# Performance work log

Hardware: AMD Instinct MI355X
Metric: run time of the kernel (lower is better)

## Reference

```python
import jax, jax.numpy as jnp
import numpy as np
from jax import lax

NCLASSES = 3
NMS_PRE = 100
NMS_THR = 0.01
SCORE_THR = 0.1
MAX_NUM = 50
H, W = 248, 216
BS = 16


def make_anchors():
    # Faithful to Anchors(ranges, sizes, rotations) in __init__.
    z0s = np.array([-0.6, -0.6, -1.78], np.float32)
    sizes = np.array([[0.6, 0.8, 1.73], [0.6, 1.76, 1.73], [1.6, 3.9, 1.56]], np.float32)
    rotations = np.array([0.0, 1.57], np.float32)
    x = (np.arange(W, dtype=np.float32) + 0.5) * (69.12 / W)
    y = (np.arange(H, dtype=np.float32) + 0.5) * (79.36 / H) - 39.68
    yy, xx = np.meshgrid(y, x, indexing='ij')  # (H, W)
    anchors = np.zeros((H, W, 3, 2, 7), np.float32)
    for c in range(3):
        for r in range(2):
            anchors[:, :, c, r, 0] = xx
            anchors[:, :, c, r, 1] = yy
            anchors[:, :, c, r, 2] = z0s[c]
            anchors[:, :, c, r, 3:6] = sizes[c]
            anchors[:, :, c, r, 6] = rotations[r]
    return jnp.asarray(anchors)


def setup_inputs() -> dict:
    key = jax.random.key(0)
    k1, k2, k3 = jax.random.split(key, 3)
    return {
        'bbox_cls_pred': jax.random.normal(k1, (BS, 18, H, W), jnp.float32),
        'bbox_pred': jax.random.normal(k2, (BS, 42, H, W), jnp.float32) * 0.1,
        'bbox_dir_cls_pred': jax.random.normal(k3, (BS, 12, H, W), jnp.float32),
        'anchors': make_anchors(),
    }


def limit_period(val, offset=1.0, period=np.pi):
    return val - jnp.floor(val / period + offset) * period


def anchors2bboxes(anchors, deltas):
    xa, ya, za, wa, la, ha, ra = [anchors[:, i] for i in range(7)]
    dx, dy, dz, dw, dl, dh, dr = [deltas[:, i] for i in range(7)]
    da = jnp.sqrt(wa * wa + la * la)
    x = dx * da + xa
    y = dy * da + ya
    z = dz * ha + za + ha * 0.5
    w = wa * jnp.exp(dw)
    l = la * jnp.exp(dl)
    h = ha * jnp.exp(dh)
    z = z - h * 0.5
    theta = ra + dr
    return jnp.stack([x, y, z, w, l, h, theta], axis=-1)


def nms_keep(boxes2d, scores, valid, thresh):
    # Greedy NMS over fixed NMS_PRE boxes; invalid boxes never kept / never suppress.
    n = scores.shape[0]
    order = jnp.argsort(-jnp.where(valid, scores, -jnp.inf))
    b = boxes2d[order]
    v = valid[order]
    area = (b[:, 2] - b[:, 0]) * (b[:, 3] - b[:, 1])
    x1 = jnp.maximum(b[:, None, 0], b[None, :, 0])
    y1 = jnp.maximum(b[:, None, 1], b[None, :, 1])
    x2 = jnp.minimum(b[:, None, 2], b[None, :, 2])
    y2 = jnp.minimum(b[:, None, 3], b[None, :, 3])
    inter = jnp.maximum(x2 - x1, 0.0) * jnp.maximum(y2 - y1, 0.0)
    iou = inter / (area[:, None] + area[None, :] - inter + 1e-8)
    idx = jnp.arange(n)
    def body(i, keep):
        sup = (iou[i] > thresh) & (idx > i) & keep[i]
        return keep & ~sup
    keep = lax.fori_loop(0, n, body, v)
    return jnp.zeros(n, bool).at[order].set(keep)


def process_single(cls_pred, box_pred, dir_pred, anchors):
    # cls_pred (18,H,W), box_pred (42,H,W), dir_pred (12,H,W), anchors (H,W,3,2,7)
    cls = jnp.transpose(cls_pred, (1, 2, 0)).reshape(-1, NCLASSES)
    box = jnp.transpose(box_pred, (1, 2, 0)).reshape(-1, 7)
    dirp = jnp.transpose(dir_pred, (1, 2, 0)).reshape(-1, 2)
    anc = anchors.reshape(-1, 7)
    cls = jax.nn.sigmoid(cls)
    dir_cls = jnp.argmax(dirp, axis=1)
    _, inds = lax.top_k(jnp.max(cls, axis=1), NMS_PRE)
    cls = cls[inds]
    box = box[inds]
    dir_cls = dir_cls[inds]
    anc = anc[inds]
    bboxes = anchors2bboxes(anc, box)  # (NMS_PRE, 7): x,y,z,w,l,h,theta
    xy = bboxes[:, :2]
    wl = bboxes[:, 3:5]
    boxes2d = jnp.concatenate([xy - wl / 2, xy + wl / 2], axis=-1)
    # Torch code detaches theta through limit_period; dir term is constant.
    theta = lax.stop_gradient(limit_period(bboxes[:, 6])) + (1.0 - dir_cls.astype(bboxes.dtype)) * np.pi
    bboxes = bboxes.at[:, 6].set(theta)
    keeps = []
    for c in range(NCLASSES):
        sc = cls[:, c]
        valid = sc > SCORE_THR
        keeps.append(nms_keep(boxes2d, sc, valid, NMS_THR) & valid)
    keep = jnp.stack(keeps)            # (3, NMS_PRE)
    scores_all = cls.T                 # (3, NMS_PRE)
    flat = jnp.where(keep, scores_all, -1.0).reshape(-1)
    final_scores, fi = lax.top_k(flat, MAX_NUM)
    sel = fi % NMS_PRE
    labels = fi // NMS_PRE
    out_bboxes = bboxes[sel]
    mask = final_scores > 0.0
    return out_bboxes, labels, final_scores, mask


def reference(bbox_cls_pred, bbox_pred, bbox_dir_cls_pred, anchors):
    f = jax.vmap(process_single, in_axes=(0, 0, 0, None))
    return f(bbox_cls_pred, bbox_pred, bbox_dir_cls_pred, anchors)
```

## Files before the change

kernel.cpp:

```cpp
#include <hip/hip_runtime.h>
#include <cstdint>

#pragma clang fp contract(off)

#define HH 248
#define WW 216
#define HW (HH*WW)
#define NROW (6*HW)
#define BATCH 16
#define NPRE 100
#define MAXNUM 50
#define NB 2048
#define CAP 2048
#define SBLK 53
#define K0 64
#define NSLOT (SBLK*K0)
#define QMAX 14
#define PIF 3.14159274101257324f

#define T0BKT 1966u
#define FBINS (NB - (int)T0BKT)

#define CNTB_OFF 0
#define KEYS_OFF 3584

__device__ __forceinline__ float sigmoidf_ref(float x) {
    if (x >= 0.0f) {
        return 1.0f / (1.0f + expf(-x));
    } else {
        float e = expf(x);
        return e / (1.0f + e);
    }
}

__device__ __forceinline__ unsigned bucket_of(unsigned bits) {
    unsigned b = (bits >= 0x3F000000u) ? (1024u + ((bits - 0x3F000000u) >> 13))
                                       : (bits >> 20);
    return (b > (unsigned)(NB - 1)) ? (unsigned)(NB - 1) : b;
}

__device__ __forceinline__ void emit_one(unsigned bits, unsigned row,
                                         unsigned* lcnt,
                                         unsigned long long* kseg) {
    if (bucket_of(bits) >= T0BKT) {
        unsigned pos = atomicAdd(lcnt, 1u);
        if (pos < (unsigned)K0)
            kseg[pos] = ((unsigned long long)bits << 32) |
                        (unsigned long long)(0xFFFFFFFFu - row);
    }
}

__global__ __launch_bounds__(256) void k_score(const float* __restrict__ cls,
                                               unsigned* __restrict__ cntB,
                                               unsigned long long* __restrict__ keys) {
    int t = threadIdx.x, blk = blockIdx.x, b = blockIdx.y;
    __shared__ unsigned lcnt;
    if (t == 0) lcnt = 0;
    __syncthreads();

    unsigned long long* kseg = keys + (size_t)(b * SBLK + blk) * K0;
    int cell0 = blk * 1024 + t * 4;
    if (cell0 < HW) {
        const float* p = cls + (size_t)b * 18 * HW;
        #pragma unroll
        for (int a = 0; a < 6; ++a) {
            float4 l0 = *(const float4*)(p + (size_t)(a*3+0)*HW + cell0);
            float4 l1 = *(const float4*)(p + (size_t)(a*3+1)*HW + cell0);
            float4 l2 = *(const float4*)(p + (size_t)(a*3+2)*HW + cell0);
            unsigned b0 = __float_as_uint(sigmoidf_ref(fmaxf(l0.x, fmaxf(l1.x, l2.x))));
            unsigned b1 = __float_as_uint(sigmoidf_ref(fmaxf(l0.y, fmaxf(l1.y, l2.y))));
            unsigned b2 = __float_as_uint(sigmoidf_ref(fmaxf(l0.z, fmaxf(l1.z, l2.z))));
            unsigned b3 = __float_as_uint(sigmoidf_ref(fmaxf(l0.w, fmaxf(l1.w, l2.w))));
            emit_one(b0, (unsigned)((cell0+0)*6 + a), &lcnt, kseg);
            emit_one(b1, (unsigned)((cell0+1)*6 + a), &lcnt, kseg);
            emit_one(b2, (unsigned)((cell0+2)*6 + a), &lcnt, kseg);
            emit_one(b3, (unsigned)((cell0+3)*6 + a), &lcnt, kseg);
        }
    }
    __syncthreads();
    if (t == 0) cntB[b * SBLK + blk] = lcnt;
}

__global__ __launch_bounds__(256) void k_final(
    const float* __restrict__ cls, const float* __restrict__ box,
    const float* __restrict__ dir, const float* __restrict__ anc,
    const unsigned* __restrict__ cntB, const unsigned long long* __restrict__ keys,
    float* __restrict__ out) {
    int b = blockIdx.x, t = threadIdx.x;

    __shared__ unsigned long long keyS[CAP];
    __shared__ int   selRow[NPRE];
    __shared__ float bb[NPRE][7];
    __shared__ float b2d[NPRE][4];
    __shared__ float areaS[NPRE];
    __shared__ float clsS[3][NPRE];
    __shared__ float svalS[3][NPRE];
    __shared__ int   ordS[3][NPRE];
    __shared__ int   rankS[3][NPRE];
    __shared__ float4 sbox[3][NPRE];
    __shared__ float  sarea[3][NPRE];
    __shared__ unsigned keepInit[3][4];
    __shared__ unsigned long long maskS[3][NPRE][2];
    __shared__ unsigned long long keepBits[3][2];
    __shared__ float flatS[3*NPRE];
    __shared__ unsigned fh[FBINS];
    __shared__ unsigned fsuf[FBINS + 1];
    __shared__ unsigned cntS[SBLK];
    __shared__ unsigned slowH[NB];
    __shared__ int  tbS;
    __shared__ unsigned StbS;
    __shared__ int  safeS;
    __shared__ unsigned mcnt;

    if (t == 0) { tbS = -1; StbS = 0; mcnt = 0; }
    if (t < FBINS) fh[t] = 0;
    if (t == FBINS) fsuf[FBINS] = 0;
    if (t < SBLK) cntS[t] = cntB[b * SBLK + t];
    __syncthreads();

    unsigned long long kq[QMAX];
    #pragma unroll
    for (int q = 0; q < QMAX; ++q) {
        unsigned long long kk = 0ULL;
        int s = t + q * 256;
        if (s < NSLOT) {
            int k = s >> 6, i = s & 63;
            if ((unsigned)i < cntS[k])
                kk = keys[(size_t)(b * SBLK + k) * K0 + i];
        }
        kq[q] = kk;
    }

    #pragma unroll
    for (int q = 0; q < QMAX; ++q) {
        unsigned bk = bucket_of((unsigned)(kq[q] >> 32));
        if (bk >= T0BKT) atomicAdd(&fh[bk - T0BKT], 1u);
    }
    __syncthreads();

    if (t < FBINS) {
        unsigned s = 0;
        int j = t;
        for (; j + 3 < FBINS; j += 4)
            s += fh[j] + fh[j+1] + fh[j+2] + fh[j+3];
        for (; j < FBINS; ++j) s += fh[j];
        fsuf[t] = s;
    }
    __syncthreads();
    if (t < FBINS) {
        unsigned S = fsuf[t], Sn = fsuf[t + 1];
        if (S >= (unsigned)NPRE && Sn < (unsigned)NPRE) {
            tbS = (int)T0BKT + t;
            StbS = S;
        }
    }
    __syncthreads();

    if (t < 64) {
        unsigned c = (t < SBLK) ? cntS[t] : 0u;
        unsigned long long ov = __ballot(c > (unsigned)K0);
        if (t == 0)
            safeS = (tbS >= 0) && (ov == 0ULL) && (StbS <= (unsigned)CAP) ? 1 : 0;
    }
    __syncthreads();

    int tb = tbS;
    int M;
    if (safeS) {
        #pragma unroll
        for (int q = 0; q < QMAX; ++q) {
            unsigned long long kk = kq[q];
            if (bucket_of((unsigned)(kk >> 32)) >= (unsigned)tb) {
                unsigned pos = atomicAdd(&mcnt, 1u);
                keyS[pos] = kk;
            }
        }
        __syncthreads();
        M = (int)mcnt;
    } else {
        for (int i = t; i < NB; i += 256) slowH[i] = 0;
        __syncthreads();
        const float* p = cls + (size_t)b * 18 * HW;
        for (int cell = t; cell < HW; cell += 256) {
            for (int a = 0; a < 6; ++a) {
                float v0 = p[(size_t)(a*3+0)*HW + cell];
                float v1 = p[(size_t)(a*3+1)*HW + cell];
                float v2 = p[(size_t)(a*3+2)*HW + cell];
                unsigned bits = __float_as_uint(sigmoidf_ref(fmaxf(v0, fmaxf(v1, v2))));
                atomicAdd(&slowH[bucket_of(bits)], 1u);
            }
        }
        __syncthreads();
        if (t == 0) {
            unsigned cum = 0;
            int r = 0;
            for (int j = NB - 1; j >= 0; --j) {
                cum += slowH[j];
                if (cum >= (unsigned)NPRE) { r = j; break; }
            }
            tbS = r;
        }
        __syncthreads();
        tb = tbS;
        for (int cell = t; cell < HW; cell += 256) {
            for (int a = 0; a < 6; ++a) {
                float v0 = p[(size_t)(a*3+0)*HW + cell];
                float v1 = p[(size_t)(a*3+1)*HW + cell];
                float v2 = p[(size_t)(a*3+2)*HW + cell];
                unsigned bits = __float_as_uint(sigmoidf_ref(fmaxf(v0, fmaxf(v1, v2))));
                if (bucket_of(bits) >= (unsigned)tb) {
                    unsigned pos = atomicAdd(&mcnt, 1u);
                    if (pos < (unsigned)CAP)
                        keyS[pos] = ((unsigned long long)bits << 32) |
                                    (unsigned long long)(0xFFFFFFFFu - (unsigned)(cell*6 + a));
                }
            }
        }
        __syncthreads();
        M = (mcnt < (unsigned)CAP) ? (int)mcnt : CAP;
    }
    __syncthreads();

    for (int i = t; i < M; i += 256) {
        unsigned long long k = keyS[i];
        int r = 0;
        int j = 0;
        for (; j + 3 < M; j += 4) {
            unsigned long long a0 = keyS[j+0], a1 = keyS[j+1];
            unsigned long long a2 = keyS[j+2], a3 = keyS[j+3];
            r += (int)(a0 > k) + (int)(a1 > k) + (int)(a2 > k) + (int)(a3 > k);
        }
        for (; j < M; ++j) r += (int)(keyS[j] > k);
        if (r < NPRE) selRow[r] = (int)(0xFFFFFFFFu - (unsigned)(k & 0xFFFFFFFFull));
    }
    __syncthreads();

    if (t < NPRE) {
        int row = selRow[t];
        int a = row % 6;
        int cell = row / 6;
        const float* cb = cls + (size_t)b * 18 * HW + cell;
        clsS[0][t] = sigmoidf_ref(cb[(size_t)(a*3+0)*HW]);
        clsS[1][t] = sigmoidf_ref(cb[(size_t)(a*3+1)*HW]);
        clsS[2][t] = sigmoidf_ref(cb[(size_t)(a*3+2)*HW]);
        const float* db = dir + (size_t)b * 12 * HW + cell;
        float d0 = db[(size_t)(a*2+0)*HW];
        float d1 = db[(size_t)(a*2+1)*HW];
        int dircls = (d1 > d0) ? 1 : 0;
        const float* pb = box + (size_t)b * 42 * HW + cell;
        float dx = pb[(size_t)(a*7+0)*HW], dy = pb[(size_t)(a*7+1)*HW], dz = pb[(size_t)(a*7+2)*HW];
        float dw = pb[(size_t)(a*7+3)*HW], dl = pb[(size_t)(a*7+4)*HW], dh = pb[(size_t)(a*7+5)*HW];
        float dr = pb[(size_t)(a*7+6)*HW];
        const float* ab = anc + (size_t)row * 7;
        float xa = ab[0], ya = ab[1], za = ab[2];
        float wa = ab[3], la = ab[4], ha = ab[5], ra = ab[6];
        float da = sqrtf(wa*wa + la*la);
        float x = dx*da + xa;
        float y = dy*da + ya;
        float z = dz*ha + za + ha*0.5f;
        float wv = wa*expf(dw);
        float lv = la*expf(dl);
        float hv = ha*expf(dh);
        z = z - hv*0.5f;
        float th0 = ra + dr;
        float lim = th0 - floorf(th0/PIF + 1.0f)*PIF;
        float theta = lim + (1.0f - (float)dircls)*PIF;
        bb[t][0]=x; bb[t][1]=y; bb[t][2]=z; bb[t][3]=wv; bb[t][4]=lv; bb[t][5]=hv; bb[t][6]=theta;
        b2d[t][0] = x - wv*0.5f;
        b2d[t][1] = y - lv*0.5f;
        b2d[t][2] = x + wv*0.5f;
        b2d[t][3] = y + lv*0.5f;
        areaS[t] = (b2d[t][2]-b2d[t][0]) * (b2d[t][3]-b2d[t][1]);
    }
    if (t < 12) keepInit[t/4][t%4] = 0u;
    __syncthreads();

    for (int w = t; w < 3*NPRE; w += 256) {
        int c = w / NPRE, p = w % NPRE;
        float sc = clsS[c][p];
        svalS[c][p] = (sc > 0.1f) ? sc : -INFINITY;
    }
    __syncthreads();

    for (int w = t; w < 3*NPRE; w += 256) {
        int c = w / NPRE, p = w % NPRE;
        float v = svalS[c][p];
        int r = 0;
        for (int j0 = 0; j0 < NPRE; j0 += 4) {
            float v0 = svalS[c][j0+0], v1 = svalS[c][j0+1];
            float v2 = svalS[c][j0+2], v3 = svalS[c][j0+3];
            r += (int)(v0 > v || (v0 == v && (j0+0) < p));
            r += (int)(v1 > v || (v1 == v && (j0+1) < p));
            r += (int)(v2 > v || (v2 == v && (j0+2) < p));
            r += (int)(v3 > v || (v3 == v && (j0+3) < p));
        }
        ordS[c][r] = p;
        rankS[c][p] = r;
        if (v != -INFINITY) atomicOr(&keepInit[c][r >> 5], 1u << (r & 31));
    }
    __syncthreads();

    for (int w = t; w < 3*NPRE; w += 256) {
        int c = w / NPRE, i = w % NPRE;
        int pi = ordS[c][i];
        sbox[c][i] = make_float4(b2d[pi][0], b2d[pi][1], b2d[pi][2], b2d[pi][3]);
        sarea[c][i] = areaS[pi];
    }
    __syncthreads();

    for (int w = t; w < 3*NPRE; w += 256) {
        int c = w / NPRE, i = w % NPRE;
        float4 bi = sbox[c][i];
        float ai = sarea[c][i];
        unsigned long long m0 = 0ULL, m1 = 0ULL;
        #pragma unroll 2
        for (int j = i + 1; j < NPRE; ++j) {
            float4 bj = sbox[c][j];
            float x1 = fmaxf(bi.x, bj.x);
            float y1 = fmaxf(bi.y, bj.y);
            float x2 = fminf(bi.z, bj.z);
            float y2 = fminf(bi.w, bj.w);
            float inter = fmaxf(x2 - x1, 0.0f) * fmaxf(y2 - y1, 0.0f);
            float iou = inter / (ai + sarea[c][j] - inter + 1e-8f);
            unsigned long long hit = (iou > 0.01f) ? 1ULL : 0ULL;
            if (j < 64) m0 |= hit << j;
            else        m1 |= hit << (j - 64);
        }
        maskS[c][i][0] = m0;
        maskS[c][i][1] = m1;
    }
    __syncthreads();

    if (t < 3) {
        int c = t;
        unsigned long long k0 = (unsigned long long)keepInit[c][0] |
                                ((unsigned long long)keepInit[c][1] << 32);
        unsigned long long k1 = (unsigned long long)keepInit[c][2] |
                                ((unsigned long long)keepInit[c][3] << 32);
        unsigned long long todo = k0;
        while (todo) {
            int i = __builtin_ctzll(todo);
            unsigned long long m0 = maskS[c][i][0];
            unsigned long long m1 = maskS[c][i][1];
            k0 &= ~m0;
            k1 &= ~m1;
            todo = (todo & (todo - 1)) & ~m0;
        }
        todo = k1;
        while (todo) {
            int i = __builtin_ctzll(todo);
            unsigned long long m1 = maskS[c][64 + i][1];
            k1 &= ~m1;
            todo = (todo & (todo - 1)) & ~m1;
        }
        keepBits[c][0] = k0;
        keepBits[c][1] = k1;
    }
    __syncthreads();

    for (int w = t; w < 3*NPRE; w += 256) {
        int c = w / NPRE, p = w % NPRE;
        int r = rankS[c][p];
        unsigned long long bit = (r < 64) ? (keepBits[c][0] >> r) : (keepBits[c][1] >> (r - 64));
        flatS[w] = (bit & 1ULL) ? clsS[c][p] : -1.0f;
    }
    __syncthreads();

    for (int i = t; i < 3*NPRE; i += 256) {
        float vi = flatS[i];
        int r2 = 0;
        for (int j0 = 0; j0 < 3*NPRE; j0 += 4) {
            float v0 = flatS[j0+0], v1 = flatS[j0+1];
            float v2 = flatS[j0+2], v3 = flatS[j0+3];
            r2 += (int)(v0 > vi || (v0 == vi && (j0+0) < i));
            r2 += (int)(v1 > vi || (v1 == vi && (j0+1) < i));
            r2 += (int)(v2 > vi || (v2 == vi && (j0+2) < i));
            r2 += (int)(v3 > vi || (v3 == vi && (j0+3) < i));
        }
        if (r2 < MAXNUM) {
            int p = i % NPRE;
            int lab = i / NPRE;
            int o = b * MAXNUM + r2;
            float* ob = out + (size_t)o * 7;
            for (int j = 0; j < 7; ++j) ob[j] = bb[p][j];
            out[BATCH*MAXNUM*7 + o] = (float)lab;
            out[BATCH*MAXNUM*8 + o] = vi;
            out[BATCH*MAXNUM*9 + o] = (vi > 0.0f) ? 1.0f : 0.0f;
        }
    }
}

extern "C" void kernel_launch(void* const* d_in, const int* in_sizes, int n_in,
                              void* d_out, int out_size, void* d_ws, size_t ws_size,
                              hipStream_t stream) {
    const float* cls = (const float*)d_in[0];
    const float* box = (const float*)d_in[1];
    const float* dir = (const float*)d_in[2];
    const float* anc = (const float*)d_in[3];
    float* out = (float*)d_out;
    char* ws = (char*)d_ws;

    unsigned* cntB = (unsigned*)(ws + CNTB_OFF);
    unsigned long long* keys = (unsigned long long*)(ws + KEYS_OFF);

    dim3 g(SBLK, BATCH);
    k_score<<<g, 256, 0, stream>>>(cls, cntB, keys);
    k_final<<<BATCH, 256, 0, stream>>>(cls, box, dir, anc, cntB, keys, out);
}
```

Before: 292.7 us.

## Fuse score scan and final NMS into one kernel with last-block election

```diff
diff --git a/kernel.cpp b/kernel.cpp
--- a/kernel.cpp
+++ b/kernel.cpp
@@ -18,10 +18,11 @@
 #define QMAX 14
 #define PIF 3.14159274101257324f
 
-#define T0BKT 1966u
-#define FBINS (NB - (int)T0BKT)
-
-#define CNTB_OFF 0
+#define XCUT 3.17805383f
+#define FBINS 92
+
+#define DONE_OFF 0
+#define CNTB_OFF 64
 #define KEYS_OFF 3584
 
 __device__ __forceinline__ float sigmoidf_ref(float x) {
@@ -39,54 +40,20 @@
     return (b > (unsigned)(NB - 1)) ? (unsigned)(NB - 1) : b;
 }
 
-__device__ __forceinline__ void emit_one(unsigned bits, unsigned row,
-                                         unsigned* lcnt,
-                                         unsigned long long* kseg) {
-    if (bucket_of(bits) >= T0BKT) {
-        unsigned pos = atomicAdd(lcnt, 1u);
-        if (pos < (unsigned)K0)
-            kseg[pos] = ((unsigned long long)bits << 32) |
-                        (unsigned long long)(0xFFFFFFFFu - row);
-    }
+__device__ __forceinline__ int lbin(unsigned bits, unsigned x0) {
+    if (bits < x0) return -1;
+    unsigned d = (bits - x0) >> 17;
+    return (d > (unsigned)(FBINS - 1)) ? (FBINS - 1) : (int)d;
 }
 
-__global__ __launch_bounds__(256) void k_score(const float* __restrict__ cls,
-                                               unsigned* __restrict__ cntB,
-                                               unsigned long long* __restrict__ keys) {
-    int t = threadIdx.x, blk = blockIdx.x, b = blockIdx.y;
-    __shared__ unsigned lcnt;
-    if (t == 0) lcnt = 0;
-    __syncthreads();
-
-    unsigned long long* kseg = keys + (size_t)(b * SBLK + blk) * K0;
-    int cell0 = blk * 1024 + t * 4;
-    if (cell0 < HW) {
-        const float* p = cls + (size_t)b * 18 * HW;
-        #pragma unroll
-        for (int a = 0; a < 6; ++a) {
-            float4 l0 = *(const float4*)(p + (size_t)(a*3+0)*HW + cell0);
-            float4 l1 = *(const float4*)(p + (size_t)(a*3+1)*HW + cell0);
-            float4 l2 = *(const float4*)(p + (size_t)(a*3+2)*HW + cell0);
-            unsigned b0 = __float_as_uint(sigmoidf_ref(fmaxf(l0.x, fmaxf(l1.x, l2.x))));
-            unsigned b1 = __float_as_uint(sigmoidf_ref(fmaxf(l0.y, fmaxf(l1.y, l2.y))));
-            unsigned b2 = __float_as_uint(sigmoidf_ref(fmaxf(l0.z, fmaxf(l1.z, l2.z))));
-            unsigned b3 = __float_as_uint(sigmoidf_ref(fmaxf(l0.w, fmaxf(l1.w, l2.w))));
-            emit_one(b0, (unsigned)((cell0+0)*6 + a), &lcnt, kseg);
-            emit_one(b1, (unsigned)((cell0+1)*6 + a), &lcnt, kseg);
-            emit_one(b2, (unsigned)((cell0+2)*6 + a), &lcnt, kseg);
-            emit_one(b3, (unsigned)((cell0+3)*6 + a), &lcnt, kseg);
-        }
-    }
-    __syncthreads();
-    if (t == 0) cntB[b * SBLK + blk] = lcnt;
-}
-
-__global__ __launch_bounds__(256) void k_final(
+__global__ __launch_bounds__(256) void k_fused(
     const float* __restrict__ cls, const float* __restrict__ box,
     const float* __restrict__ dir, const float* __restrict__ anc,
-    const unsigned* __restrict__ cntB, const unsigned long long* __restrict__ keys,
+    unsigned* __restrict__ doneCnt, unsigned* __restrict__ cntB,
+    unsigned long long* __restrict__ keys,
     float* __restrict__ out) {
-    int b = blockIdx.x, t = threadIdx.x;
+    int t = threadIdx.x, blk = blockIdx.x, b = blockIdx.y;
+    const unsigned x0 = __float_as_uint(XCUT);
 
     __shared__ unsigned long long keyS[CAP];
     __shared__ int   selRow[NPRE];
@@ -111,6 +78,62 @@
     __shared__ unsigned StbS;
     __shared__ int  safeS;
     __shared__ unsigned mcnt;
+    __shared__ unsigned lcnt;
+    __shared__ int  amLastS;
+
+    if (t == 0) lcnt = 0;
+    __syncthreads();
+
+    unsigned long long* kseg = keys + (size_t)(b * SBLK + blk) * K0;
+    int cell0 = blk * 1024 + t * 4;
+    if (cell0 < HW) {
+        const float* p = cls + (size_t)b * 18 * HW;
+        #pragma unroll
+        for (int a = 0; a < 6; ++a) {
+            float4 l0 = *(const float4*)(p + (size_t)(a*3+0)*HW + cell0);
+            float4 l1 = *(const float4*)(p + (size_t)(a*3+1)*HW + cell0);
+            float4 l2 = *(const float4*)(p + (size_t)(a*3+2)*HW + cell0);
+            float m0 = fmaxf(l0.x, fmaxf(l1.x, l2.x));
+            float m1 = fmaxf(l0.y, fmaxf(l1.y, l2.y));
+            float m2 = fmaxf(l0.z, fmaxf(l1.z, l2.z));
+            float m3 = fmaxf(l0.w, fmaxf(l1.w, l2.w));
+            if (m0 >= XCUT) {
+                unsigned pos = atomicAdd(&lcnt, 1u);
+                if (pos < (unsigned)K0)
+                    kseg[pos] = ((unsigned long long)__float_as_uint(m0) << 32) |
+                                (unsigned long long)(0xFFFFFFFFu - (unsigned)((cell0+0)*6 + a));
+            }
+            if (m1 >= XCUT) {
+                unsigned pos = atomicAdd(&lcnt, 1u);
+                if (pos < (unsigned)K0)
+                    kseg[pos] = ((unsigned long long)__float_as_uint(m1) << 32) |
+                                (unsigned long long)(0xFFFFFFFFu - (unsigned)((cell0+1)*6 + a));
+            }
+            if (m2 >= XCUT) {
+                unsigned pos = atomicAdd(&lcnt, 1u);
+                if (pos < (unsigned)K0)
+                    kseg[pos] = ((unsigned long long)__float_as_uint(m2) << 32) |
+                                (unsigned long long)(0xFFFFFFFFu - (unsigned)((cell0+2)*6 + a));
+            }
+            if (m3 >= XCUT) {
+                unsigned pos = atomicAdd(&lcnt, 1u);
+                if (pos < (unsigned)K0)
+                    kseg[pos] = ((unsigned long long)__float_as_uint(m3) << 32) |
+                                (unsigned long long)(0xFFFFFFFFu - (unsigned)((cell0+3)*6 + a));
+            }
+        }
+    }
+    __syncthreads();
+    if (t == 0) cntB[b * SBLK + blk] = lcnt;
+
+    __threadfence();
+    if (t == 0) {
+        unsigned done = atomicAdd(&doneCnt[b], 1u);
+        amLastS = (done == (unsigned)(SBLK - 1)) ? 1 : 0;
+    }
+    __syncthreads();
+    if (!amLastS) return;
+    __threadfence();
 
     if (t == 0) { tbS = -1; StbS = 0; mcnt = 0; }
     if (t < FBINS) fh[t] = 0;
@@ -133,8 +156,8 @@
 
     #pragma unroll
     for (int q = 0; q < QMAX; ++q) {
-        unsigned bk = bucket_of((unsigned)(kq[q] >> 32));
-        if (bk >= T0BKT) atomicAdd(&fh[bk - T0BKT], 1u);
+        int bk = lbin((unsigned)(kq[q] >> 32), x0);
+        if (bk >= 0) atomicAdd(&fh[bk], 1u);
     }
     __syncthreads();
 
@@ -150,7 +173,7 @@
     if (t < FBINS) {
         unsigned S = fsuf[t], Sn = fsuf[t + 1];
         if (S >= (unsigned)NPRE && Sn < (unsigned)NPRE) {
-            tbS = (int)T0BKT + t;
+            tbS = t;
             StbS = S;
         }
     }
@@ -164,13 +187,13 @@
     }
     __syncthreads();
 
-    int tb = tbS;
     int M;
     if (safeS) {
+        int tbin = tbS;
         #pragma unroll
         for (int q = 0; q < QMAX; ++q) {
             unsigned long long kk = kq[q];
-            if (bucket_of((unsigned)(kk >> 32)) >= (unsigned)tb) {
+            if (lbin((unsigned)(kk >> 32), x0) >= tbin) {
                 unsigned pos = atomicAdd(&mcnt, 1u);
                 keyS[pos] = kk;
             }
@@ -201,7 +224,7 @@
             tbS = r;
         }
         __syncthreads();
-        tb = tbS;
+        int tb = tbS;
         for (int cell = t; cell < HW; cell += 256) {
             for (int a = 0; a < 6; ++a) {
                 float v0 = p[(size_t)(a*3+0)*HW + cell];
@@ -400,10 +423,12 @@
     float* out = (float*)d_out;
     char* ws = (char*)d_ws;
 
+    unsigned* doneCnt = (unsigned*)(ws + DONE_OFF);
     unsigned* cntB = (unsigned*)(ws + CNTB_OFF);
     unsigned long long* keys = (unsigned long long*)(ws + KEYS_OFF);
 
+    hipMemsetAsync(doneCnt, 0, 64, stream);
+
     dim3 g(SBLK, BATCH);
-    k_score<<<g, 256, 0, stream>>>(cls, cntB, keys);
-    k_final<<<BATCH, 256, 0, stream>>>(cls, box, dir, anc, cntB, keys, out);
+    k_fused<<<g, 256, 0, stream>>>(cls, box, dir, anc, doneCnt, cntB, keys, out);
 }
```

Result: slower. 394.2 us (+34.7%).
